# Kernel optimization log

Measured on AMD Instinct MI355X. Metric: run time of the kernel, lower is better.

## Reference

```python
import jax, jax.numpy as jnp
import numpy as np

ROI_SIZE = 7
CROP = ROI_SIZE * 2  # tf crop_and_resize target before 2x2 maxpool


def crop_and_resize(img, boxes, size):
    """TF-semantics bilinear crop_and_resize for a single image.
    img: [H, W, C]; boxes: [N, 4] normalized (y1, x1, y2, x2). -> [N, size, size, C]
    """
    H, W, C = img.shape
    y1, x1, y2, x2 = boxes[:, 0], boxes[:, 1], boxes[:, 2], boxes[:, 3]
    i = jnp.arange(size, dtype=boxes.dtype)
    # TF: in_y = y1*(H-1) + i*(y2-y1)*(H-1)/(size-1)
    ys = y1[:, None] * (H - 1) + i[None, :] * ((y2 - y1)[:, None] * (H - 1) / (size - 1))  # [N,S]
    xs = x1[:, None] * (W - 1) + i[None, :] * ((x2 - x1)[:, None] * (W - 1) / (size - 1))  # [N,S]
    y0 = jnp.floor(ys)
    x0 = jnp.floor(xs)
    wy = (ys - y0)[:, :, None, None]  # [N,S,1,1]
    wx = (xs - x0)[:, None, :, None]  # [N,1,S,1]
    y0i = jnp.clip(y0.astype(jnp.int32), 0, H - 1)
    y1i = jnp.clip(y0i + 1, 0, H - 1)
    x0i = jnp.clip(x0.astype(jnp.int32), 0, W - 1)
    x1i = jnp.clip(x0i + 1, 0, W - 1)

    def gather(yi, xi):  # [N,S],[N,S] -> [N,S,S,C]
        return img[yi[:, :, None], xi[:, None, :]]

    top = gather(y0i, x0i) * (1 - wx) + gather(y0i, x1i) * wx
    bot = gather(y1i, x0i) * (1 - wx) + gather(y1i, x1i) * wx
    return top * (1 - wy) + bot * wy


def setup_inputs() -> dict:
    key = jax.random.key(0)
    ks = jax.random.split(key, 10)
    feats = jax.random.uniform(ks[0], (1, 38, 50, 512), dtype=jnp.float32)  # relu-like feature map
    # valid normalized boxes: sort endpoints per axis
    yy = jnp.sort(jax.random.uniform(ks[1], (1000, 2), dtype=jnp.float32), axis=1)
    xx = jnp.sort(jax.random.uniform(ks[2], (1000, 2), dtype=jnp.float32), axis=1)
    proposals = jnp.stack([yy[:, 0], xx[:, 0], yy[:, 1], xx[:, 1]], axis=1)  # [N,4] y1,x1,y2,x2
    d_flat = ROI_SIZE * ROI_SIZE * 512  # 25088
    W1 = jax.random.normal(ks[3], (d_flat, 4096), dtype=jnp.float32) * 0.01
    b1 = jnp.zeros((4096,), jnp.float32)
    W2 = jax.random.normal(ks[4], (4096, 4096), dtype=jnp.float32) * 0.01
    b2 = jnp.zeros((4096,), jnp.float32)
    Wc = jax.random.normal(ks[5], (4096, 21), dtype=jnp.float32) * 0.01  # class head, stddev 0.01
    bc = jnp.zeros((21,), jnp.float32)
    Wr = jax.random.normal(ks[6], (4096, 80), dtype=jnp.float32) * 0.001  # reg head, stddev 0.001
    br = jnp.zeros((80,), jnp.float32)
    return {"feats": feats, "proposals": proposals, "W1": W1, "b1": b1, "W2": W2,
            "b2": b2, "Wc": Wc, "bc": bc, "Wr": Wr, "br": br}


def reference(feats, proposals, W1, b1, W2, b2, Wc, bc, Wr, br):
    # roi_pool: crop_and_resize to 14x14 (batch_idx all 0), then 2x2 maxpool stride 2 -> 7x7
    rois = crop_and_resize(feats[0], proposals, CROP)  # [N,14,14,C]
    N, _, _, C = rois.shape
    pooled = rois.reshape(N, ROI_SIZE, 2, ROI_SIZE, 2, C).max(axis=(2, 4))  # [N,7,7,C]
    x = pooled.reshape(N, -1)  # flatten (row-major, matches keras Flatten on NHWC)
    x = jax.nn.relu(x @ W1 + b1)
    x = jax.nn.relu(x @ W2 + b2)
    cls_out = jax.nn.softmax(x @ Wc + bc, axis=-1)          # [N, num_classes]
    reg_out = (x @ Wr + br).reshape(N, -1, 4)               # [N, num_classes-1, 4]
    return cls_out, reg_out
```

## Files before the change

kernel.cpp:

```cpp
#include <hip/hip_runtime.h>
#include <stdint.h>

typedef __bf16 bf16x8 __attribute__((ext_vector_type(8)));
typedef float f32x16 __attribute__((ext_vector_type(16)));
typedef float f32x4 __attribute__((ext_vector_type(4)));

__device__ __forceinline__ unsigned short f2bf(float f) {
    unsigned int u = __float_as_uint(f);
    unsigned int r = (u + 0x7fffu + ((u >> 16) & 1u)) >> 16;
    return (unsigned short)r;
}
__device__ __forceinline__ float bf2f(unsigned int h) {
    return __uint_as_float(h << 16);
}

__device__ __forceinline__ void gld_lds16(const void* g, void* l) {
    __builtin_amdgcn_global_load_lds((const __attribute__((address_space(1))) void*)g,
                                     (__attribute__((address_space(3))) void*)l, 16, 0, 0);
}

__global__ __launch_bounds__(256) void k_cvt_feats(const float* __restrict__ src,
                                                   unsigned short* __restrict__ dst) {
    int g = blockIdx.x * 256 + threadIdx.x;
    float4 v = ((const float4*)src)[g];
    ushort4 o;
    o.x = f2bf(v.x); o.y = f2bf(v.y); o.z = f2bf(v.z); o.w = f2bf(v.w);
    ((ushort4*)dst)[g] = o;
}

__global__ __launch_bounds__(256) void k_roipool(const unsigned short* __restrict__ feats,
                                                 const float* __restrict__ props,
                                                 unsigned short* __restrict__ pooled) {
    int b = blockIdx.x;
    int r = b / 49;
    int cell = b - r * 49;
    int py = cell / 7, px = cell - py * 7;
    int c = threadIdx.x * 2;
    unsigned int* outp = (unsigned int*)(pooled + (size_t)r * 25088 + cell * 512 + c);
    if (r >= 1000) { *outp = 0u; return; }
    float y1 = props[r * 4 + 0], x1 = props[r * 4 + 1];
    float y2 = props[r * 4 + 2], x2 = props[r * 4 + 3];
    float sy = (y2 - y1) * (37.0f / 13.0f);
    float sx = (x2 - x1) * (49.0f / 13.0f);
    float m0 = -1e30f, m1 = -1e30f;
#pragma unroll
    for (int a = 0; a < 2; ++a) {
        float ys = y1 * 37.0f + (float)(2 * py + a) * sy;
        float y0f = floorf(ys);
        float wy = ys - y0f;
        int y0 = (int)y0f; y0 = min(max(y0, 0), 37);
        int y1i = min(y0 + 1, 37);
#pragma unroll
        for (int bb = 0; bb < 2; ++bb) {
            float xs = x1 * 49.0f + (float)(2 * px + bb) * sx;
            float x0f = floorf(xs);
            float wx = xs - x0f;
            int x0 = (int)x0f; x0 = min(max(x0, 0), 49);
            int x1i = min(x0 + 1, 49);
            unsigned int t00 = *(const unsigned int*)(feats + ((y0 * 50 + x0) * 512 + c));
            unsigned int t01 = *(const unsigned int*)(feats + ((y0 * 50 + x1i) * 512 + c));
            unsigned int t10 = *(const unsigned int*)(feats + ((y1i * 50 + x0) * 512 + c));
            unsigned int t11 = *(const unsigned int*)(feats + ((y1i * 50 + x1i) * 512 + c));
            float w00 = (1.f - wy) * (1.f - wx), w01 = (1.f - wy) * wx;
            float w10 = wy * (1.f - wx), w11 = wy * wx;
            float v0 = bf2f(t00 & 0xffffu) * w00 + bf2f(t01 & 0xffffu) * w01 +
                       bf2f(t10 & 0xffffu) * w10 + bf2f(t11 & 0xffffu) * w11;
            float v1 = bf2f(t00 >> 16) * w00 + bf2f(t01 >> 16) * w01 +
                       bf2f(t10 >> 16) * w10 + bf2f(t11 >> 16) * w11;
            m0 = fmaxf(m0, v0);
            m1 = fmaxf(m1, v1);
        }
    }
    *outp = ((unsigned int)f2bf(m1) << 16) | (unsigned int)f2bf(m0);
}

__global__ __launch_bounds__(256) void k_transpose_cvt(const float* __restrict__ B,
                                                       unsigned short* __restrict__ BT,
                                                       int K, int N) {
    __shared__ unsigned int tile[64][32];
    int k0 = blockIdx.x * 64;
    int n0 = blockIdx.y * 64;
    int t = threadIdx.x;
    int kr = (t >> 4) * 2;
    int c4 = (t & 15) * 4;
#pragma unroll
    for (int ii = 0; ii < 2; ++ii) {
        int k = kr + ii * 32;
        int kd = k >> 1;
        const float* p0 = B + (size_t)(k0 + k) * N + n0 + c4;
        float4 v0 = *(const float4*)p0;
        float4 v1 = *(const float4*)(p0 + N);
        float lo[4] = {v0.x, v0.y, v0.z, v0.w};
        float hi[4] = {v1.x, v1.y, v1.z, v1.w};
#pragma unroll
        for (int c = 0; c < 4; ++c) {
            int n = c4 + c;
            int dw = (((kd >> 1) ^ ((n >> 2) & 7)) << 1) | (kd & 1);
            tile[n][dw] = (unsigned)f2bf(lo[c]) | ((unsigned)f2bf(hi[c]) << 16);
        }
    }
    __syncthreads();
    int nl = t >> 2;
    int x = (nl >> 2) & 7;
    int pbase = (t & 3) * 4;
    uint2 r[4];
#pragma unroll
    for (int q = 0; q < 4; ++q) {
        int p = (pbase + q) ^ x;
        r[q] = *(const uint2*)&tile[nl][p << 1];
    }
    unsigned short* dst = BT + (size_t)(n0 + nl) * K + k0 + (t & 3) * 16;
    uint4 o0, o1;
    o0.x = r[0].x; o0.y = r[0].y; o0.z = r[1].x; o0.w = r[1].y;
    o1.x = r[2].x; o1.y = r[2].y; o1.z = r[3].x; o1.w = r[3].y;
    *(uint4*)(dst + 0) = o0;
    *(uint4*)(dst + 8) = o1;
}

__global__ __launch_bounds__(512, 2) void k_gemm256(const unsigned short* __restrict__ A,
                                                    const unsigned short* __restrict__ BT,
                                                    float* __restrict__ Cpart,
                                                    int N, int K, int kChunk, int MN) {
    __shared__ __align__(16) char lds[131072];
    const int n0 = blockIdx.x * 256;
    const int m0 = blockIdx.y * 256;
    const int kBeg = blockIdx.z * kChunk;
    const int NT = kChunk >> 6;
    const int t = threadIdx.x;
    const int l = t & 63;
    const int wave = t >> 6;
    const int wrow = wave >> 2;
    const int wcol = wave & 3;
    const int l15 = l & 15;
    const int lq = l >> 4;
    const size_t rK = (size_t)K;

    const int rowoff = l15 * 128;
    const int cb0 = ((lq ^ (l & 7)) << 4);
    const int cb1 = (((4 + lq) ^ (l & 7)) << 4);

    const int srow = t >> 3;
    const int sj = (t & 7) ^ (srow & 7);
    const unsigned short* agp = A + (size_t)(m0 + srow) * rK + sj * 8;
    const unsigned short* bgp = BT + (size_t)(n0 + srow) * rK + sj * 8;
    char* aldst = (char*)lds + t * 16;
    char* bldst = (char*)lds + 32768 + t * 16;

#define STAGE_A(bi, h, kt) do {                                                           \
        gld_lds16(agp + (size_t)((h) * 128) * rK + (kt), aldst + (bi) * 65536 + (h) * 16384);        \
        gld_lds16(agp + (size_t)((h) * 128 + 64) * rK + (kt), aldst + (bi) * 65536 + (h) * 16384 + 8192); \
    } while (0)
#define STAGE_B(bi, h, kt) do {                                                           \
        gld_lds16(bgp + (size_t)((h) * 128) * rK + (kt), bldst + (bi) * 65536 + (h) * 16384);        \
        gld_lds16(bgp + (size_t)((h) * 128 + 64) * rK + (kt), bldst + (bi) * 65536 + (h) * 16384 + 8192); \
    } while (0)

    f32x4 acc[8][4];
#pragma unroll
    for (int i = 0; i < 8; ++i)
#pragma unroll
        for (int j = 0; j < 4; ++j) acc[i][j] = (f32x4){0.f, 0.f, 0.f, 0.f};

    bf16x8 bB[4][2];
    bf16x8 aA[2][2];

    STAGE_A(0, 0, kBeg); STAGE_A(0, 1, kBeg);
    STAGE_B(0, 0, kBeg); STAGE_B(0, 1, kBeg);
    STAGE_B(1, 0, kBeg + 64); STAGE_B(1, 1, kBeg + 64);
    asm volatile("s_waitcnt vmcnt(4)" ::: "memory");
    __builtin_amdgcn_s_barrier();

    int cur = 0;
    for (int tt = 0; tt < NT; ++tt) {
        const char* Ab = (const char*)lds + cur * 65536 + wrow * 16384 + rowoff;
        const char* Bb = (const char*)lds + cur * 65536 + 32768 + wcol * 8192 + rowoff;
        const int nx = cur ^ 1;
        const bool tn1 = (tt + 1 < NT);
        const bool tn2 = (tt + 2 < NT);
        const int k1 = kBeg + (tt + 1) * 64;
        const int k2 = kBeg + (tt + 2) * 64;
#pragma unroll
        for (int q = 0; q < 4; ++q) {
            aA[0][0] = *(const bf16x8*)(Ab + (2 * q) * 2048 + cb0);
            aA[0][1] = *(const bf16x8*)(Ab + (2 * q) * 2048 + cb1);
            aA[1][0] = *(const bf16x8*)(Ab + (2 * q + 1) * 2048 + cb0);
            aA[1][1] = *(const bf16x8*)(Ab + (2 * q + 1) * 2048 + cb1);
            if (q == 0) {
#pragma unroll
                for (int nf = 0; nf < 4; ++nf) {
                    bB[nf][0] = *(const bf16x8*)(Bb + nf * 2048 + cb0);
                    bB[nf][1] = *(const bf16x8*)(Bb + nf * 2048 + cb1);
                }
            }
            if (q == 0) { if (tn1) STAGE_A(nx, 0, k1); }
            if (q == 1) { if (tn1) STAGE_A(nx, 1, k1); }
            if (q == 2) { if (tn2) STAGE_B(cur, 0, k2); }
            if (q == 3) {
                if (tn2) {
                    STAGE_B(cur, 1, k2);
                    asm volatile("s_waitcnt vmcnt(4)" ::: "memory");
                } else {
                    asm volatile("s_waitcnt vmcnt(0)" ::: "memory");
                }
            }
            __builtin_amdgcn_s_barrier();
            asm volatile("s_waitcnt lgkmcnt(0)" ::: "memory");
            __builtin_amdgcn_s_setprio(1);
#pragma unroll
            for (int kh = 0; kh < 2; ++kh)
#pragma unroll
                for (int nf = 0; nf < 4; ++nf) {
                    acc[2 * q][nf] = __builtin_amdgcn_mfma_f32_16x16x32_bf16(
                        aA[0][kh], bB[nf][kh], acc[2 * q][nf], 0, 0, 0);
                    acc[2 * q + 1][nf] = __builtin_amdgcn_mfma_f32_16x16x32_bf16(
                        aA[1][kh], bB[nf][kh], acc[2 * q + 1][nf], 0, 0, 0);
                }
            __builtin_amdgcn_s_setprio(0);
            __builtin_amdgcn_s_barrier();
        }
        cur = nx;
    }
#undef STAGE_A
#undef STAGE_B

    float* Cp = Cpart + (size_t)blockIdx.z * MN;
    const int row0 = m0 + wrow * 128 + lq * 4;
    const int col0 = n0 + wcol * 64 + l15;
#pragma unroll
    for (int mf = 0; mf < 8; ++mf)
#pragma unroll
        for (int r = 0; r < 4; ++r) {
            float* p = Cp + (size_t)(row0 + mf * 16 + r) * N + col0;
            p[0]  = acc[mf][0][r];
            p[16] = acc[mf][1][r];
            p[32] = acc[mf][2][r];
            p[48] = acc[mf][3][r];
        }
}

__global__ __launch_bounds__(256) void k_gemm(const unsigned short* __restrict__ A,
                                              const unsigned short* __restrict__ BT,
                                              float* __restrict__ Cpart,
                                              int N, int K, int kChunk, int MN) {
    __shared__ __align__(16) unsigned short As[128 * 64];
    __shared__ __align__(16) unsigned short Bs[128 * 64];
    const int n0 = blockIdx.x * 128;
    const int m0 = blockIdx.y * 128;
    const int kBeg = blockIdx.z * kChunk;
    const int kEnd = kBeg + kChunk;
    const int t = threadIdx.x;
    const int lane = t & 63;
    const int wave = t >> 6;
    const int wm = (wave & 1) * 64;
    const int wn = (wave >> 1) * 64;
    const int l31 = lane & 31;
    const int half = lane >> 5;
    const int xorb = l31 & 7;

    const int srow = t >> 3;
    const int sj = (t & 7) ^ (srow & 7);
    const unsigned short* ag = A + (size_t)(m0 + srow) * K + sj * 8;
    const unsigned short* bg = BT + (size_t)(n0 + srow) * K + sj * 8;
    char* alb = (char*)As + t * 16;
    char* blb = (char*)Bs + t * 16;
    const int rq = K * 32;

    f32x16 acc[2][2] = {};
    const unsigned short* aBase = As + (wm + l31) * 64;
    const unsigned short* bBase = Bs + (wn + l31) * 64;

    for (int kt = kBeg; kt < kEnd; kt += 64) {
#pragma unroll
        for (int q = 0; q < 4; ++q) gld_lds16(ag + kt + q * rq, alb + q * 4096);
#pragma unroll
        for (int q = 0; q < 4; ++q) gld_lds16(bg + kt + q * rq, blb + q * 4096);
        __syncthreads();
#pragma unroll
        for (int s = 0; s < 4; ++s) {
            const int off = ((s * 2 + half) ^ xorb) * 8;
            bf16x8 a0 = *(const bf16x8*)(aBase + off);
            bf16x8 a1 = *(const bf16x8*)(aBase + 2048 + off);
            bf16x8 b0 = *(const bf16x8*)(bBase + off);
            bf16x8 b1 = *(const bf16x8*)(bBase + 2048 + off);
            acc[0][0] = __builtin_amdgcn_mfma_f32_32x32x16_bf16(a0, b0, acc[0][0], 0, 0, 0);
            acc[0][1] = __builtin_amdgcn_mfma_f32_32x32x16_bf16(a0, b1, acc[0][1], 0, 0, 0);
            acc[1][0] = __builtin_amdgcn_mfma_f32_32x32x16_bf16(a1, b0, acc[1][0], 0, 0, 0);
            acc[1][1] = __builtin_amdgcn_mfma_f32_32x32x16_bf16(a1, b1, acc[1][1], 0, 0, 0);
        }
        __syncthreads();
    }

    float* Cp = Cpart + (size_t)blockIdx.z * MN;
    const int colb = n0 + wn + l31;
    const int rbase = m0 + wm + 4 * half;
#pragma unroll
    for (int i = 0; i < 2; ++i)
#pragma unroll
        for (int j = 0; j < 2; ++j)
#pragma unroll
            for (int reg = 0; reg < 16; ++reg) {
                int row = rbase + i * 32 + (reg & 3) + 8 * (reg >> 2);
                Cp[(size_t)row * N + colb + j * 32] = acc[i][j][reg];
            }
}

__global__ __launch_bounds__(256) void k_bias_relu_cvt(const float* __restrict__ accP,
                                                       const float* __restrict__ bias,
                                                       unsigned short* __restrict__ out) {
    int gI = blockIdx.x * 256 + threadIdx.x;
    const float4* p = (const float4*)accP;
    float4 v0 = p[gI];
    float4 v1 = p[gI + 1048576];
    float4 v2 = p[gI + 2097152];
    float4 v3 = p[gI + 3145728];
    float4 b = ((const float4*)bias)[gI & 1023];
    ushort4 o;
    o.x = f2bf(fmaxf(v0.x + v1.x + v2.x + v3.x + b.x, 0.f));
    o.y = f2bf(fmaxf(v0.y + v1.y + v2.y + v3.y + b.y, 0.f));
    o.z = f2bf(fmaxf(v0.z + v1.z + v2.z + v3.z + b.z, 0.f));
    o.w = f2bf(fmaxf(v0.w + v1.w + v2.w + v3.w + b.w, 0.f));
    ((ushort4*)out)[gI] = o;
}

__global__ __launch_bounds__(256) void k_pack_w3(const float* __restrict__ Wc,
                                                 const float* __restrict__ Wr,
                                                 unsigned short* __restrict__ W3T) {
    int gI = blockIdx.x * 256 + threadIdx.x;
    int n = gI >> 12, k = gI & 4095;
    float v = 0.f;
    if (n < 21) v = Wc[k * 21 + n];
    else if (n < 101) v = Wr[k * 80 + (n - 21)];
    W3T[gI] = f2bf(v);
}

__global__ __launch_bounds__(64) void k_head(const float* __restrict__ acc3,
                                             const float* __restrict__ bc,
                                             const float* __restrict__ br,
                                             float* __restrict__ out) {
    int r = blockIdx.x;
    int lane = threadIdx.x;
    float logit = -1e30f;
    if (lane < 21) {
        logit = bc[lane];
#pragma unroll
        for (int z = 0; z < 16; ++z) logit += acc3[z * 131072 + r * 128 + lane];
    }
    float mx = logit;
#pragma unroll
    for (int m = 32; m >= 1; m >>= 1) mx = fmaxf(mx, __shfl_xor(mx, m, 64));
    float e = (lane < 21) ? expf(logit - mx) : 0.f;
    float s = e;
#pragma unroll
    for (int m = 32; m >= 1; m >>= 1) s += __shfl_xor(s, m, 64);
    if (lane < 21) out[r * 21 + lane] = e / s;
    for (int j = lane; j < 80; j += 64) {
        float v = br[j];
#pragma unroll
        for (int z = 0; z < 16; ++z) v += acc3[z * 131072 + r * 128 + 21 + j];
        out[21000 + r * 80 + j] = v;
    }
}

extern "C" void kernel_launch(void* const* d_in, const int* in_sizes, int n_in,
                              void* d_out, int out_size, void* d_ws, size_t ws_size,
                              hipStream_t stream) {
    (void)in_sizes; (void)n_in; (void)out_size; (void)ws_size;
    const float* feats = (const float*)d_in[0];
    const float* props = (const float*)d_in[1];
    const float* W1    = (const float*)d_in[2];
    const float* b1    = (const float*)d_in[3];
    const float* W2    = (const float*)d_in[4];
    const float* b2    = (const float*)d_in[5];
    const float* Wc    = (const float*)d_in[6];
    const float* bc    = (const float*)d_in[7];
    const float* Wr    = (const float*)d_in[8];
    const float* br    = (const float*)d_in[9];
    float* out = (float*)d_out;

    char* ws = (char*)d_ws;
    unsigned short* W1T    = (unsigned short*)ws; ws += (size_t)4096 * 25088 * 2;
    unsigned short* W2T    = (unsigned short*)ws; ws += (size_t)4096 * 4096 * 2;
    unsigned short* W3T    = (unsigned short*)ws; ws += (size_t)128 * 4096 * 2;
    unsigned short* featsb = (unsigned short*)ws; ws += (size_t)972800 * 2;
    unsigned short* pooled = (unsigned short*)ws; ws += (size_t)1024 * 25088 * 2;
    unsigned short* x1     = (unsigned short*)ws; ws += (size_t)1024 * 4096 * 2;
    unsigned short* x2     = (unsigned short*)ws; ws += (size_t)1024 * 4096 * 2;
    float* accP            = (float*)ws;          ws += (size_t)4 * 1024 * 4096 * 4;
    float* acc3P           = accP;

    k_cvt_feats<<<950, 256, 0, stream>>>(feats, featsb);
    k_roipool<<<1024 * 49, 256, 0, stream>>>(featsb, props, pooled);
    k_transpose_cvt<<<dim3(392, 64), 256, 0, stream>>>(W1, W1T, 25088, 4096);
    k_gemm256<<<dim3(16, 4, 4), 512, 0, stream>>>(pooled, W1T, accP, 4096, 25088, 6272, 1024 * 4096);
    k_bias_relu_cvt<<<4096, 256, 0, stream>>>(accP, b1, x1);
    k_transpose_cvt<<<dim3(64, 64), 256, 0, stream>>>(W2, W2T, 4096, 4096);
    k_gemm256<<<dim3(16, 4, 4), 512, 0, stream>>>(x1, W2T, accP, 4096, 4096, 1024, 1024 * 4096);
    k_bias_relu_cvt<<<4096, 256, 0, stream>>>(accP, b2, x2);
    k_pack_w3<<<2048, 256, 0, stream>>>(Wc, Wr, W3T);
    k_gemm<<<dim3(1, 8, 16), 256, 0, stream>>>(x2, W3T, acc3P, 128, 4096, 256, 1024 * 128);
    k_head<<<1000, 64, 0, stream>>>(acc3P, bc, br, out);
}
```

Before: 932.0 us.

## Enlarge transpose tiles, batch ROI cells per block, deepen head split-K

```diff
diff --git a/kernel.cpp b/kernel.cpp
--- a/kernel.cpp
+++ b/kernel.cpp
@@ -31,90 +31,93 @@
 __global__ __launch_bounds__(256) void k_roipool(const unsigned short* __restrict__ feats,
                                                  const float* __restrict__ props,
                                                  unsigned short* __restrict__ pooled) {
-    int b = blockIdx.x;
-    int r = b / 49;
-    int cell = b - r * 49;
-    int py = cell / 7, px = cell - py * 7;
+    int r = blockIdx.x >> 1;
+    int par = blockIdx.x & 1;
     int c = threadIdx.x * 2;
-    unsigned int* outp = (unsigned int*)(pooled + (size_t)r * 25088 + cell * 512 + c);
-    if (r >= 1000) { *outp = 0u; return; }
+    unsigned short* outr = pooled + (size_t)r * 25088 + c;
+    if (r >= 1000) {
+        for (int cell = par; cell < 49; cell += 2) *(unsigned int*)(outr + cell * 512) = 0u;
+        return;
+    }
     float y1 = props[r * 4 + 0], x1 = props[r * 4 + 1];
     float y2 = props[r * 4 + 2], x2 = props[r * 4 + 3];
     float sy = (y2 - y1) * (37.0f / 13.0f);
     float sx = (x2 - x1) * (49.0f / 13.0f);
-    float m0 = -1e30f, m1 = -1e30f;
-#pragma unroll
-    for (int a = 0; a < 2; ++a) {
-        float ys = y1 * 37.0f + (float)(2 * py + a) * sy;
-        float y0f = floorf(ys);
-        float wy = ys - y0f;
-        int y0 = (int)y0f; y0 = min(max(y0, 0), 37);
-        int y1i = min(y0 + 1, 37);
-#pragma unroll
-        for (int bb = 0; bb < 2; ++bb) {
-            float xs = x1 * 49.0f + (float)(2 * px + bb) * sx;
-            float x0f = floorf(xs);
-            float wx = xs - x0f;
-            int x0 = (int)x0f; x0 = min(max(x0, 0), 49);
-            int x1i = min(x0 + 1, 49);
-            unsigned int t00 = *(const unsigned int*)(feats + ((y0 * 50 + x0) * 512 + c));
-            unsigned int t01 = *(const unsigned int*)(feats + ((y0 * 50 + x1i) * 512 + c));
-            unsigned int t10 = *(const unsigned int*)(feats + ((y1i * 50 + x0) * 512 + c));
-            unsigned int t11 = *(const unsigned int*)(feats + ((y1i * 50 + x1i) * 512 + c));
-            float w00 = (1.f - wy) * (1.f - wx), w01 = (1.f - wy) * wx;
-            float w10 = wy * (1.f - wx), w11 = wy * wx;
-            float v0 = bf2f(t00 & 0xffffu) * w00 + bf2f(t01 & 0xffffu) * w01 +
-                       bf2f(t10 & 0xffffu) * w10 + bf2f(t11 & 0xffffu) * w11;
-            float v1 = bf2f(t00 >> 16) * w00 + bf2f(t01 >> 16) * w01 +
-                       bf2f(t10 >> 16) * w10 + bf2f(t11 >> 16) * w11;
-            m0 = fmaxf(m0, v0);
-            m1 = fmaxf(m1, v1);
+    for (int cell = par; cell < 49; cell += 2) {
+        int py = cell / 7, px = cell - py * 7;
+        float m0 = -1e30f, m1 = -1e30f;
+#pragma unroll
+        for (int a = 0; a < 2; ++a) {
+            float ys = y1 * 37.0f + (float)(2 * py + a) * sy;
+            float y0f = floorf(ys);
+            float wy = ys - y0f;
+            int y0 = (int)y0f; y0 = min(max(y0, 0), 37);
+            int y1i = min(y0 + 1, 37);
+#pragma unroll
+            for (int bb = 0; bb < 2; ++bb) {
+                float xs = x1 * 49.0f + (float)(2 * px + bb) * sx;
+                float x0f = floorf(xs);
+                float wx = xs - x0f;
+                int x0 = (int)x0f; x0 = min(max(x0, 0), 49);
+                int x1i = min(x0 + 1, 49);
+                unsigned int t00 = *(const unsigned int*)(feats + ((y0 * 50 + x0) * 512 + c));
+                unsigned int t01 = *(const unsigned int*)(feats + ((y0 * 50 + x1i) * 512 + c));
+                unsigned int t10 = *(const unsigned int*)(feats + ((y1i * 50 + x0) * 512 + c));
+                unsigned int t11 = *(const unsigned int*)(feats + ((y1i * 50 + x1i) * 512 + c));
+                float w00 = (1.f - wy) * (1.f - wx), w01 = (1.f - wy) * wx;
+                float w10 = wy * (1.f - wx), w11 = wy * wx;
+                float v0 = bf2f(t00 & 0xffffu) * w00 + bf2f(t01 & 0xffffu) * w01 +
+                           bf2f(t10 & 0xffffu) * w10 + bf2f(t11 & 0xffffu) * w11;
+                float v1 = bf2f(t00 >> 16) * w00 + bf2f(t01 >> 16) * w01 +
+                           bf2f(t10 >> 16) * w10 + bf2f(t11 >> 16) * w11;
+                m0 = fmaxf(m0, v0);
+                m1 = fmaxf(m1, v1);
+            }
         }
-    }
-    *outp = ((unsigned int)f2bf(m1) << 16) | (unsigned int)f2bf(m0);
+        *(unsigned int*)(outr + cell * 512) =
+            ((unsigned int)f2bf(m1) << 16) | (unsigned int)f2bf(m0);
+    }
 }
 
 __global__ __launch_bounds__(256) void k_transpose_cvt(const float* __restrict__ B,
                                                        unsigned short* __restrict__ BT,
                                                        int K, int N) {
-    __shared__ unsigned int tile[64][32];
-    int k0 = blockIdx.x * 64;
-    int n0 = blockIdx.y * 64;
+    __shared__ unsigned int tile[128][16][4];
+    int k0 = blockIdx.x * 128;
+    int n0 = blockIdx.y * 128;
     int t = threadIdx.x;
-    int kr = (t >> 4) * 2;
-    int c4 = (t & 15) * 4;
-#pragma unroll
-    for (int ii = 0; ii < 2; ++ii) {
-        int k = kr + ii * 32;
-        int kd = k >> 1;
-        const float* p0 = B + (size_t)(k0 + k) * N + n0 + c4;
-        float4 v0 = *(const float4*)p0;
-        float4 v1 = *(const float4*)(p0 + N);
-        float lo[4] = {v0.x, v0.y, v0.z, v0.w};
-        float hi[4] = {v1.x, v1.y, v1.z, v1.w};
-#pragma unroll
-        for (int c = 0; c < 4; ++c) {
-            int n = c4 + c;
-            int dw = (((kd >> 1) ^ ((n >> 2) & 7)) << 1) | (kd & 1);
-            tile[n][dw] = (unsigned)f2bf(lo[c]) | ((unsigned)f2bf(hi[c]) << 16);
+    int rpb = t >> 4;
+    int cgb = t & 15;
+#pragma unroll
+    for (int itr = 0; itr < 4; ++itr) {
+        int rp = rpb + itr * 16;
+        const float* prow = B + (size_t)(k0 + rp * 2) * N + n0;
+#pragma unroll
+        for (int itc = 0; itc < 2; ++itc) {
+            int cg = cgb + itc * 16;
+            const float* p0 = prow + cg * 4;
+            float4 v0 = *(const float4*)p0;
+            float4 v1 = *(const float4*)(p0 + N);
+            float lo[4] = {v0.x, v0.y, v0.z, v0.w};
+            float hi[4] = {v1.x, v1.y, v1.z, v1.w};
+#pragma unroll
+            for (int cc = 0; cc < 4; ++cc) {
+                int n = cg * 4 + cc;
+                int p = (rp >> 2) ^ (n & 15);
+                tile[n][p][rp & 3] = (unsigned)f2bf(lo[cc]) | ((unsigned)f2bf(hi[cc]) << 16);
+            }
         }
     }
     __syncthreads();
-    int nl = t >> 2;
-    int x = (nl >> 2) & 7;
-    int pbase = (t & 3) * 4;
-    uint2 r[4];
-#pragma unroll
-    for (int q = 0; q < 4; ++q) {
-        int p = (pbase + q) ^ x;
-        r[q] = *(const uint2*)&tile[nl][p << 1];
-    }
-    unsigned short* dst = BT + (size_t)(n0 + nl) * K + k0 + (t & 3) * 16;
-    uint4 o0, o1;
-    o0.x = r[0].x; o0.y = r[0].y; o0.z = r[1].x; o0.w = r[1].y;
-    o1.x = r[2].x; o1.y = r[2].y; o1.z = r[3].x; o1.w = r[3].y;
-    *(uint4*)(dst + 0) = o0;
-    *(uint4*)(dst + 8) = o1;
+    int j = t & 15;
+    int nb = t >> 4;
+#pragma unroll
+    for (int it = 0; it < 8; ++it) {
+        int n = nb + it * 16;
+        int p = j ^ (n & 15);
+        uint4 o = *(const uint4*)&tile[n][p][0];
+        *(uint4*)(BT + (size_t)(n0 + n) * K + k0 + j * 8) = o;
+    }
 }
 
 __global__ __launch_bounds__(512, 2) void k_gemm256(const unsigned short* __restrict__ A,
@@ -343,7 +346,7 @@
     if (lane < 21) {
         logit = bc[lane];
 #pragma unroll
-        for (int z = 0; z < 16; ++z) logit += acc3[z * 131072 + r * 128 + lane];
+        for (int z = 0; z < 32; ++z) logit += acc3[z * 131072 + r * 128 + lane];
     }
     float mx = logit;
 #pragma unroll
@@ -356,7 +359,7 @@
     for (int j = lane; j < 80; j += 64) {
         float v = br[j];
 #pragma unroll
-        for (int z = 0; z < 16; ++z) v += acc3[z * 131072 + r * 128 + 21 + j];
+        for (int z = 0; z < 32; ++z) v += acc3[z * 131072 + r * 128 + 21 + j];
         out[21000 + r * 80 + j] = v;
     }
 }
@@ -389,14 +392,14 @@
     float* acc3P           = accP;
 
     k_cvt_feats<<<950, 256, 0, stream>>>(feats, featsb);
-    k_roipool<<<1024 * 49, 256, 0, stream>>>(featsb, props, pooled);
-    k_transpose_cvt<<<dim3(392, 64), 256, 0, stream>>>(W1, W1T, 25088, 4096);
+    k_roipool<<<2048, 256, 0, stream>>>(featsb, props, pooled);
+    k_transpose_cvt<<<dim3(196, 32), 256, 0, stream>>>(W1, W1T, 25088, 4096);
     k_gemm256<<<dim3(16, 4, 4), 512, 0, stream>>>(pooled, W1T, accP, 4096, 25088, 6272, 1024 * 4096);
     k_bias_relu_cvt<<<4096, 256, 0, stream>>>(accP, b1, x1);
-    k_transpose_cvt<<<dim3(64, 64), 256, 0, stream>>>(W2, W2T, 4096, 4096);
+    k_transpose_cvt<<<dim3(32, 32), 256, 0, stream>>>(W2, W2T, 4096, 4096);
     k_gemm256<<<dim3(16, 4, 4), 512, 0, stream>>>(x1, W2T, accP, 4096, 4096, 1024, 1024 * 4096);
     k_bias_relu_cvt<<<4096, 256, 0, stream>>>(accP, b2, x2);
     k_pack_w3<<<2048, 256, 0, stream>>>(Wc, Wr, W3T);
-    k_gemm<<<dim3(1, 8, 16), 256, 0, stream>>>(x2, W3T, acc3P, 128, 4096, 256, 1024 * 128);
+    k_gemm<<<dim3(1, 8, 32), 256, 0, stream>>>(x2, W3T, acc3P, 128, 4096, 128, 1024 * 128);
     k_head<<<1000, 64, 0, stream>>>(acc3P, bc, br, out);
 }
```

Result: no change. 944.9 us (+1.4%).
